# Kernel tuning notes

Hardware: AMD Instinct MI355X
Metric: run time of the kernel (lower is better)

## Reference

```python
import jax, jax.numpy as jnp
import numpy as np

B, L = 4, 2048
D_MODEL, D_STATE, D_CONV, EXPAND = 1024, 16, 4, 2
D_INNER = D_MODEL * EXPAND


def setup_inputs() -> dict:
    key = jax.random.key(0)
    ks = jax.random.split(key, 6)
    x = jax.random.normal(ks[0], (B, L, D_MODEL), dtype=jnp.float32)
    W_in = jax.random.normal(ks[1], (D_MODEL, 2 * D_INNER), dtype=jnp.float32) / np.sqrt(D_MODEL)
    conv_w = jax.random.normal(ks[2], (D_INNER, D_CONV), dtype=jnp.float32) / np.sqrt(D_CONV)
    conv_b = jax.random.normal(ks[3], (D_INNER,), dtype=jnp.float32) * 0.02
    W_x = jax.random.normal(ks[4], (D_INNER, 2 * D_STATE + 1), dtype=jnp.float32) / np.sqrt(D_INNER)
    A_log = jnp.log(jnp.arange(1, D_STATE + 1, dtype=jnp.float32))
    D_param = jnp.ones((D_INNER,), dtype=jnp.float32)
    W_out = jax.random.normal(ks[5], (D_INNER, D_MODEL), dtype=jnp.float32) / np.sqrt(D_INNER)
    return {"x": x, "W_in": W_in, "conv_w": conv_w, "conv_b": conv_b,
            "W_x": W_x, "A_log": A_log, "D_param": D_param, "W_out": W_out}


def _silu(v):
    return v * jax.nn.sigmoid(v)


def reference(x, W_in, conv_w, conv_b, W_x, A_log, D_param, W_out):
    b, l, _ = x.shape
    # input projection and split into ssm branch and gate
    xz = x @ W_in                                   # (b, l, 2*d_inner)
    x_ssm, z = jnp.split(xz, 2, axis=-1)            # each (b, l, d_inner)
    # depthwise causal conv1d (kernel D_CONV, left pad D_CONV-1, truncate to l)
    xp = jnp.pad(x_ssm, ((0, 0), (D_CONV - 1, 0), (0, 0)))
    xc = conv_b
    for k in range(D_CONV):                         # small fixed kernel loop
        xc = xc + xp[:, k:k + l, :] * conv_w[:, k]
    xc = _silu(xc)                                  # (b, l, d_inner)
    # input-dependent delta, B, C
    x_dbl = xc @ W_x                                # (b, l, 2*d_state+1)
    delta = jax.nn.softplus(x_dbl[..., :1])         # (b, l, 1)
    B_mat = x_dbl[..., 1:1 + D_STATE]               # (b, l, n)
    C_mat = x_dbl[..., 1 + D_STATE:]                # (b, l, n)
    A = -jnp.exp(A_log)                             # (n,)
    A_bar = jnp.exp(delta * A)                      # (b, l, n)
    B_bar = delta * B_mat                           # (b, l, n)

    def step(h, inp):
        a, bb, xt, ct = inp                         # (b,n),(b,n),(b,d),(b,n)
        h = a[:, None, :] * h + bb[:, None, :] * xt[:, :, None]  # (b,d,n)
        y = jnp.einsum('bdn,bn->bd', h, ct)
        return h, y

    h0 = jnp.zeros((b, D_INNER, D_STATE), dtype=x.dtype)
    seq = (jnp.swapaxes(A_bar, 0, 1), jnp.swapaxes(B_bar, 0, 1),
           jnp.swapaxes(xc, 0, 1), jnp.swapaxes(C_mat, 0, 1))
    _, ys = jax.lax.scan(step, h0, seq)             # (l, b, d_inner)
    y = jnp.swapaxes(ys, 0, 1)
    y = y + xc * D_param                            # skip connection
    y = y * _silu(z)                                # gating
    return y @ W_out                                # (b, l, d_model)
```

## Files before the change

kernel.cpp:

```cpp
#include <hip/hip_runtime.h>
#include <hip/hip_bf16.h>
#include <math.h>

typedef __hip_bfloat16 bf16;
typedef __attribute__((ext_vector_type(8))) short short8;
typedef __attribute__((ext_vector_type(4))) float f32x4;

#define BATCH   4
#define L_SEQ   2048
#define DMODEL  1024
#define DSTATE  16
#define DCONV   4
#define DINNER  2048
#define M_ROWS  (BATCH * L_SEQ)

#define CHUNK   64
#define NCH     (L_SEQ / CHUNK)
#define PSTR    52
#define NX      33

__device__ __forceinline__ float b2f(bf16 v) { return __bfloat162float(v); }
__device__ __forceinline__ bf16  f2b(float v) { return __float2bfloat16(v); }
__device__ __forceinline__ float us2f(unsigned short u) {
    return __uint_as_float(((unsigned)u) << 16);
}
__device__ __forceinline__ float ldany(const void* p, int i, int f32) {
    return f32 ? ((const float*)p)[i] : b2f(((const bf16*)p)[i]);
}
__device__ __forceinline__ void load_lds16(const void* g, void* l) {
    __builtin_amdgcn_global_load_lds(
        (const __attribute__((address_space(1))) unsigned int*)g,
        (__attribute__((address_space(3))) unsigned int*)l, 16, 0, 0);
}

union V8 { float4 f4; unsigned short us[8]; };

__global__ void detect_dtype(const unsigned int* __restrict__ alog_bits,
                             int* __restrict__ flag)
{
    *flag = (alog_bits[0] == 0u) ? 1 : 0;
}

__global__ __launch_bounds__(256) void convert_bf16(
    const void* __restrict__ src, bf16* __restrict__ dst, int n,
    const int* __restrict__ flag)
{
    const int f = *flag;
    int i = blockIdx.x * 256 + threadIdx.x;
    if (i < n) dst[i] = f2b(ldany(src, i, f));
}

__global__ __launch_bounds__(256) void transpose_any(
    const void* __restrict__ src, bf16* __restrict__ dst,
    int R, int C, const int* __restrict__ flag)
{
    const int f = *flag;
    __shared__ float tile[32][33];
    int tx = threadIdx.x & 31;
    int ty = threadIdx.x >> 5;
    int c0 = blockIdx.x * 32;
    int r0 = blockIdx.y * 32;
    #pragma unroll
    for (int i = 0; i < 4; i++) {
        int r = r0 + ty + i * 8;
        tile[ty + i * 8][tx] = ldany(src, r * C + c0 + tx, f);
    }
    __syncthreads();
    #pragma unroll
    for (int i = 0; i < 4; i++) {
        int cr = c0 + ty + i * 8;
        dst[(size_t)cr * R + r0 + tx] = f2b(tile[tx][ty + i * 8]);
    }
}

__global__ __launch_bounds__(256) void gemm_mfma(
    const bf16* __restrict__ A, const bf16* __restrict__ Bt,
    void* __restrict__ C1, void* __restrict__ C2,
    int M, int N, int K, int split,
    const int* __restrict__ flag, int oMode)
{
    const int fo = (oMode == 2) ? 1 : (oMode & *flag);
    __shared__ __align__(16) bf16 As[128 * 32];
    __shared__ __align__(16) bf16 Bs[128 * 32];
    const int tid  = threadIdx.x;
    const int lane = tid & 63;
    const int w    = tid >> 6;
    const int wr   = w & 1, wc = w >> 1;
    const int m0   = blockIdx.y * 128;
    const int n0   = blockIdx.x * 128;

    f32x4 acc[4][4] = {};

    const int ldr = lane >> 2;
    const int ldc = (lane & 3) * 8;
    const int mrow = lane & 15;
    const int qk   = (lane >> 4) * 8;

    for (int k0 = 0; k0 < K; k0 += 32) {
        __syncthreads();
        #pragma unroll
        for (int j = 0; j < 2; j++) {
            int rg = w * 2 + j;
            int r  = rg * 16 + ldr;
            load_lds16(A  + (size_t)(m0 + r) * K + k0 + ldc, (char*)As + rg * 1024);
            load_lds16(Bt + (size_t)(n0 + r) * K + k0 + ldc, (char*)Bs + rg * 1024);
        }
        __syncthreads();

        short8 af[4], bfr[4];
        #pragma unroll
        for (int i = 0; i < 4; i++) {
            af[i]  = *(const short8*)&As[(wr * 64 + i * 16 + mrow) * 32 + qk];
            bfr[i] = *(const short8*)&Bs[(wc * 64 + i * 16 + mrow) * 32 + qk];
        }
        #pragma unroll
        for (int mi = 0; mi < 4; mi++)
            #pragma unroll
            for (int ni = 0; ni < 4; ni++)
                acc[mi][ni] = __builtin_amdgcn_mfma_f32_16x16x32_bf16(
                    af[mi], bfr[ni], acc[mi][ni], 0, 0, 0);
    }

    const int orow = wr * 64 + (lane >> 4) * 4;
    const int ocol = wc * 64 + (lane & 15);
    #pragma unroll
    for (int mi = 0; mi < 4; mi++)
        #pragma unroll
        for (int ni = 0; ni < 4; ni++)
            #pragma unroll
            for (int r = 0; r < 4; r++) {
                int row = m0 + orow + mi * 16 + r;
                int col = n0 + ocol + ni * 16;
                if (col >= N) continue;
                float v = acc[mi][ni][r];
                if (col < split) {
                    if (fo) ((float*)C1)[(size_t)row * split + col] = v;
                    else    ((bf16*)C1)[(size_t)row * split + col]  = f2b(v);
                } else {
                    int c2 = col - split;
                    if (fo) ((float*)C2)[(size_t)row * (N - split) + c2] = v;
                    else    ((bf16*)C2)[(size_t)row * (N - split) + c2]  = f2b(v);
                }
            }
}

#define CLC 16

__global__ __launch_bounds__(256) void conv_silu_kernel(
    const bf16* __restrict__ x_ssm, const void* __restrict__ conv_w,
    const void* __restrict__ conv_b, bf16* __restrict__ xc,
    const int* __restrict__ flag)
{
    const int f   = *flag;
    const int tid = threadIdx.x;
    const int d0  = tid * 8;
    const int b   = blockIdx.x / (L_SEQ / CLC);
    const int l0  = (blockIdx.x % (L_SEQ / CLC)) * CLC;

    float wk[DCONV][8], bias[8];
    #pragma unroll
    for (int j = 0; j < 8; j++) {
        bias[j] = ldany(conv_b, d0 + j, f);
        #pragma unroll
        for (int k = 0; k < DCONV; k++)
            wk[k][j] = ldany(conv_w, (d0 + j) * DCONV + k, f);
    }

    const size_t rowstr = DINNER;
    const unsigned short* xin = (const unsigned short*)x_ssm;

    float win[3][8];
    #pragma unroll
    for (int r = 0; r < 3; r++) {
        int l = l0 - 3 + r;
        if (l >= 0) {
            V8 v; v.f4 = *(const float4*)(xin + ((size_t)(b * L_SEQ + l)) * rowstr + d0);
            #pragma unroll
            for (int j = 0; j < 8; j++) win[r][j] = us2f(v.us[j]);
        } else {
            #pragma unroll
            for (int j = 0; j < 8; j++) win[r][j] = 0.f;
        }
    }

    #pragma unroll
    for (int t = 0; t < CLC; t++) {
        int l = l0 + t;
        V8 v; v.f4 = *(const float4*)(xin + ((size_t)(b * L_SEQ + l)) * rowstr + d0);
        float cur[8];
        #pragma unroll
        for (int j = 0; j < 8; j++) cur[j] = us2f(v.us[j]);

        V8 o;
        #pragma unroll
        for (int j = 0; j < 8; j++) {
            float s = bias[j];
            s = fmaf(wk[0][j], win[0][j], s);
            s = fmaf(wk[1][j], win[1][j], s);
            s = fmaf(wk[2][j], win[2][j], s);
            s = fmaf(wk[3][j], cur[j],    s);
            float sv = s / (1.f + __expf(-s));
            o.us[j] = (unsigned short)(__bfloat16_as_ushort(f2b(sv)));
        }
        *(float4*)((unsigned short*)xc + ((size_t)(b * L_SEQ + l)) * rowstr + d0) = o.f4;

        #pragma unroll
        for (int j = 0; j < 8; j++) {
            win[0][j] = win[1][j];
            win[1][j] = win[2][j];
            win[2][j] = cur[j];
        }
    }
}

__global__ void transpose_wx(const void* __restrict__ W_x, bf16* __restrict__ W_xT,
                             const int* __restrict__ flag)
{
    const int f = *flag;
    int idx = blockIdx.x * 256 + threadIdx.x;
    if (idx >= NX * DINNER) return;
    int n = idx / DINNER;
    int k = idx - n * DINNER;
    W_xT[idx] = f2b(ldany(W_x, k * NX + n, f));
}

__global__ __launch_bounds__(256) void pack_P(
    const float* __restrict__ xdbl, const void* __restrict__ A_log,
    float* __restrict__ P, const int* __restrict__ flag)
{
    const int f = *flag;
    int i  = blockIdx.x * 256 + threadIdx.x;
    int bl = i >> 4, n = i & 15;
    const float* row = xdbl + (size_t)bl * NX;
    float x0 = row[0];
    float delta = (x0 > 20.f) ? x0 : log1pf(expf(x0));
    float Aneg = -expf(ldany(A_log, n, f));
    float* p = P + (size_t)bl * PSTR;
    p[n]      = expf(delta * Aneg);
    p[16 + n] = delta * row[1 + n];
    p[32 + n] = row[17 + n];
    if (n == 0) p[48] = delta;
}

__global__ __launch_bounds__(256) void scan_phase1(
    const float* __restrict__ P, const bf16* __restrict__ xc,
    float* __restrict__ hstate)
{
    const int blk = blockIdx.x;
    const int b = blk >> 8;
    const int c = (blk >> 3) & 31;
    const int g = blk & 7;
    const int tid = threadIdx.x;
    const int d = g * 256 + tid;

    __shared__ __align__(16) float sP[CHUNK][PSTR];
    __shared__ __align__(16) unsigned short sX[CHUNK][256];

    const float4* psrc = (const float4*)(P + ((size_t)(b * L_SEQ) + c * CHUNK) * PSTR);
    float4* pdst = (float4*)&sP[0][0];
    #pragma unroll
    for (int r = 0; r < 4; r++) {
        int i = r * 256 + tid;
        if (i < (CHUNK * PSTR) / 4) pdst[i] = psrc[i];
    }
    #pragma unroll
    for (int r = 0; r < 16; r++) {
        int i = r * 256 + tid;
        int t = i >> 6;
        int dd = (i & 63) * 4;
        *(ushort4*)&sX[t][dd] = *(const ushort4*)((const unsigned short*)xc +
            ((size_t)(b * L_SEQ) + c * CHUNK + t) * DINNER + g * 256 + dd);
    }
    __syncthreads();

    float h[16];
    #pragma unroll
    for (int n = 0; n < 16; n++) h[n] = 0.f;

    for (int t = 0; t < CHUNK; t++) {
        float xv = us2f(sX[t][tid]);
        float4 a0 = *(const float4*)&sP[t][0];
        float4 a1 = *(const float4*)&sP[t][4];
        float4 a2 = *(const float4*)&sP[t][8];
        float4 a3 = *(const float4*)&sP[t][12];
        float4 b0 = *(const float4*)&sP[t][16];
        float4 b1 = *(const float4*)&sP[t][20];
        float4 b2 = *(const float4*)&sP[t][24];
        float4 b3 = *(const float4*)&sP[t][28];
        float av[16] = {a0.x,a0.y,a0.z,a0.w, a1.x,a1.y,a1.z,a1.w,
                        a2.x,a2.y,a2.z,a2.w, a3.x,a3.y,a3.z,a3.w};
        float bv[16] = {b0.x,b0.y,b0.z,b0.w, b1.x,b1.y,b1.z,b1.w,
                        b2.x,b2.y,b2.z,b2.w, b3.x,b3.y,b3.z,b3.w};
        #pragma unroll
        for (int n = 0; n < 16; n++)
            h[n] = fmaf(av[n], h[n], bv[n] * xv);
    }
    float* out = hstate + (((size_t)b * NCH + c) * DINNER + d) * 16;
    #pragma unroll
    for (int q = 0; q < 4; q++)
        *(float4*)&out[q * 4] = *(const float4*)&h[q * 4];
}

__global__ void sum_delta(const float* __restrict__ P, float* __restrict__ S)
{
    int i = threadIdx.x;
    const float* p = P + ((size_t)((i >> 5) * L_SEQ) + (i & 31) * CHUNK) * PSTR + 48;
    float s = 0.f;
    for (int t = 0; t < CHUNK; t++) s += p[(size_t)t * PSTR];
    S[i] = s;
}

__global__ __launch_bounds__(256) void scan_phase2(
    float* __restrict__ hstate, const float* __restrict__ S,
    const void* __restrict__ A_log, const int* __restrict__ flag)
{
    const int f = *flag;
    const int b = blockIdx.x >> 7;
    const int dg = blockIdx.x & 127;
    const int tid = threadIdx.x;
    const int d = dg * 16 + (tid >> 4);
    const int n = tid & 15;
    const float Aneg = -expf(ldany(A_log, n, f));

    __shared__ float sS[NCH];
    if (tid < NCH) sS[tid] = S[b * NCH + tid];
    __syncthreads();

    float H = 0.f;
    size_t base = ((size_t)b * NCH * DINNER + d) * 16 + n;
    for (int c = 0; c < NCH; c++) {
        size_t idx = base + (size_t)c * (DINNER * 16);
        float hend = hstate[idx];
        hstate[idx] = H;
        H = fmaf(__expf(Aneg * sS[c]), H, hend);
    }
}

__global__ __launch_bounds__(256) void scan_phase3(
    const float* __restrict__ P, const bf16* __restrict__ xc,
    const bf16* __restrict__ z, const void* __restrict__ Dp,
    const float* __restrict__ hstate, bf16* __restrict__ y,
    const int* __restrict__ flag)
{
    const int f = *flag;
    const int blk = blockIdx.x;
    const int b = blk >> 8;
    const int c = (blk >> 3) & 31;
    const int g = blk & 7;
    const int tid = threadIdx.x;
    const int d = g * 256 + tid;

    __shared__ __align__(16) float sP[CHUNK][PSTR];
    __shared__ __align__(16) unsigned short sX[CHUNK][256];

    const float4* psrc = (const float4*)(P + ((size_t)(b * L_SEQ) + c * CHUNK) * PSTR);
    float4* pdst = (float4*)&sP[0][0];
    #pragma unroll
    for (int r = 0; r < 4; r++) {
        int i = r * 256 + tid;
        if (i < (CHUNK * PSTR) / 4) pdst[i] = psrc[i];
    }
    #pragma unroll
    for (int r = 0; r < 16; r++) {
        int i = r * 256 + tid;
        int t = i >> 6;
        int dd = (i & 63) * 4;
        *(ushort4*)&sX[t][dd] = *(const ushort4*)((const unsigned short*)xc +
            ((size_t)(b * L_SEQ) + c * CHUNK + t) * DINNER + g * 256 + dd);
    }
    __syncthreads();

    const float Dd = ldany(Dp, d, f);
    float h[16];
    const float* hin = hstate + (((size_t)b * NCH + c) * DINNER + d) * 16;
    #pragma unroll
    for (int q = 0; q < 4; q++)
        *(float4*)&h[q * 4] = *(const float4*)&hin[q * 4];

    const size_t ybase = ((size_t)(b * L_SEQ) + c * CHUNK) * DINNER + d;
    const unsigned short* zp = (const unsigned short*)z;

    #pragma unroll 4
    for (int t = 0; t < CHUNK; t++) {
        float xv = us2f(sX[t][tid]);
        float4 a0 = *(const float4*)&sP[t][0];
        float4 a1 = *(const float4*)&sP[t][4];
        float4 a2 = *(const float4*)&sP[t][8];
        float4 a3 = *(const float4*)&sP[t][12];
        float4 b0 = *(const float4*)&sP[t][16];
        float4 b1 = *(const float4*)&sP[t][20];
        float4 b2 = *(const float4*)&sP[t][24];
        float4 b3 = *(const float4*)&sP[t][28];
        float4 c0 = *(const float4*)&sP[t][32];
        float4 c1 = *(const float4*)&sP[t][36];
        float4 c2 = *(const float4*)&sP[t][40];
        float4 c3 = *(const float4*)&sP[t][44];
        float av[16] = {a0.x,a0.y,a0.z,a0.w, a1.x,a1.y,a1.z,a1.w,
                        a2.x,a2.y,a2.z,a2.w, a3.x,a3.y,a3.z,a3.w};
        float bv[16] = {b0.x,b0.y,b0.z,b0.w, b1.x,b1.y,b1.z,b1.w,
                        b2.x,b2.y,b2.z,b2.w, b3.x,b3.y,b3.z,b3.w};
        float cv[16] = {c0.x,c0.y,c0.z,c0.w, c1.x,c1.y,c1.z,c1.w,
                        c2.x,c2.y,c2.z,c2.w, c3.x,c3.y,c3.z,c3.w};
        float p0 = 0.f, p1 = 0.f;
        #pragma unroll
        for (int n = 0; n < 16; n += 2) {
            h[n]     = fmaf(av[n],     h[n],     bv[n]     * xv);
            h[n + 1] = fmaf(av[n + 1], h[n + 1], bv[n + 1] * xv);
            p0 = fmaf(h[n],     cv[n],     p0);
            p1 = fmaf(h[n + 1], cv[n + 1], p1);
        }
        float zv = us2f(zp[ybase + (size_t)t * DINNER]);
        float yv = (p0 + p1) + xv * Dd;
        float sz = zv / (1.f + __expf(-zv));
        y[ybase + (size_t)t * DINNER] = f2b(yv * sz);
    }
}

extern "C" void kernel_launch(void* const* d_in, const int* in_sizes, int n_in,
                              void* d_out, int out_size, void* d_ws, size_t ws_size,
                              hipStream_t stream)
{
    const void* x      = d_in[0];
    const void* W_in   = d_in[1];
    const void* conv_w = d_in[2];
    const void* conv_b = d_in[3];
    const void* W_x    = d_in[4];
    const void* A_log  = d_in[5];
    const void* Dp     = d_in[6];
    const void* W_out  = d_in[7];

    char* w = (char*)d_ws;
    bf16* x_ssm = (bf16*)w; w += (size_t)M_ROWS * DINNER * 2;
    bf16* z     = (bf16*)w; w += (size_t)M_ROWS * DINNER * 2;
    bf16* xc    = (bf16*)w; w += (size_t)M_ROWS * DINNER * 2;
    bf16* yb    = (bf16*)w; w += (size_t)M_ROWS * DINNER * 2;
    float* P    = (float*)w; w += (size_t)M_ROWS * PSTR * 4;
    int*  flag  = (int*)w;  w += 256;
    float* S    = (float*)w; w += 4096;

    bf16* x_bf    = yb;
    bf16* W_inT   = xc;
    bf16* W_outT  = x_ssm;
    float* hstate = (float*)((char*)x_ssm + (size_t)DMODEL * DINNER * 2);
    float* xdbl  = (float*)yb;
    bf16*  W_xT  = (bf16*)((char*)yb + 2 * 1024 * 1024);

    detect_dtype<<<1, 1, 0, stream>>>((const unsigned int*)A_log, flag);

    convert_bf16<<<(M_ROWS * DMODEL) / 256, 256, 0, stream>>>(x, x_bf, M_ROWS * DMODEL, flag);
    transpose_any<<<dim3((2 * DINNER) / 32, DMODEL / 32), 256, 0, stream>>>(
        W_in, W_inT, DMODEL, 2 * DINNER, flag);

    gemm_mfma<<<dim3((2 * DINNER) / 128, M_ROWS / 128), 256, 0, stream>>>(
        x_bf, W_inT, x_ssm, z, M_ROWS, 2 * DINNER, DMODEL, DINNER, flag, 0);

    conv_silu_kernel<<<BATCH * (L_SEQ / CLC), 256, 0, stream>>>(
        x_ssm, conv_w, conv_b, xc, flag);

    transpose_any<<<dim3(DMODEL / 32, DINNER / 32), 256, 0, stream>>>(
        W_out, W_outT, DINNER, DMODEL, flag);

    transpose_wx<<<(NX * DINNER + 255) / 256, 256, 0, stream>>>(W_x, W_xT, flag);
    gemm_mfma<<<dim3(1, M_ROWS / 128), 256, 0, stream>>>(
        xc, W_xT, xdbl, xdbl, M_ROWS, NX, DINNER, NX, flag, 2);
    pack_P<<<(M_ROWS * 16) / 256, 256, 0, stream>>>(xdbl, A_log, P, flag);

    scan_phase1<<<BATCH * NCH * 8, 256, 0, stream>>>(P, xc, hstate);
    sum_delta<<<1, BATCH * NCH, 0, stream>>>(P, S);
    scan_phase2<<<BATCH * 128, 256, 0, stream>>>(hstate, S, A_log, flag);
    scan_phase3<<<BATCH * NCH * 8, 256, 0, stream>>>(P, xc, z, Dp, hstate, yb, flag);

    gemm_mfma<<<dim3(DMODEL / 128, M_ROWS / 128), 256, 0, stream>>>(
        yb, W_outT, d_out, d_out, M_ROWS, DMODEL, DINNER, DMODEL, flag, 1);
}
```

Baseline: 454.2 us.

## Split-K the x_dbl GEMM, read scan params from global, parallelize delta sums

The narrow xc@W_x GEMM now splits K four ways into separate fp32 partial buffers, and pack_P sums the partials, so 256 blocks run instead of 64. The scan kernels drop the LDS staging of the per-step parameter rows and read them directly from global memory, which is broadcast across the block. sum_delta becomes one wavefront per chunk with a shuffle reduction, and the GEMM epilogue gets fast paths for tiles that fall wholly on one side of the split. The split-K path adds partial-buffer traffic and an extra reduction, and the global broadcast reads depend on cache behaviour.

After: 408.7 us. 10.0% less time.

```diff
diff --git a/kernel.cpp b/kernel.cpp
--- a/kernel.cpp
+++ b/kernel.cpp
@@ -18,6 +18,7 @@
 #define NCH     (L_SEQ / CHUNK)
 #define PSTR    52
 #define NX      33
+#define KSPL    4
 
 __device__ __forceinline__ float b2f(bf16 v) { return __bfloat162float(v); }
 __device__ __forceinline__ bf16  f2b(float v) { return __float2bfloat16(v); }
@@ -75,9 +76,9 @@
 
 __global__ __launch_bounds__(256) void gemm_mfma(
     const bf16* __restrict__ A, const bf16* __restrict__ Bt,
-    void* __restrict__ C1, void* __restrict__ C2,
-    int M, int N, int K, int split,
-    const int* __restrict__ flag, int oMode)
+    void* __restrict__ C1v, void* __restrict__ C2v,
+    int M, int N, int Kfull, int split,
+    const int* __restrict__ flag, int oMode, int K)
 {
     const int fo = (oMode == 2) ? 1 : (oMode & *flag);
     __shared__ __align__(16) bf16 As[128 * 32];
@@ -88,6 +89,12 @@
     const int wr   = w & 1, wc = w >> 1;
     const int m0   = blockIdx.y * 128;
     const int n0   = blockIdx.x * 128;
+    const int kz   = blockIdx.z;
+    const int kst  = kz * K;
+
+    void* C1 = C1v;
+    void* C2 = C2v;
+    if (kz) { C1 = (char*)C1v + (size_t)kz * M * N * 4; C2 = C1; }
 
     f32x4 acc[4][4] = {};
 
@@ -96,14 +103,14 @@
     const int mrow = lane & 15;
     const int qk   = (lane >> 4) * 8;
 
-    for (int k0 = 0; k0 < K; k0 += 32) {
+    for (int k0 = kst; k0 < kst + K; k0 += 32) {
         __syncthreads();
         #pragma unroll
         for (int j = 0; j < 2; j++) {
             int rg = w * 2 + j;
             int r  = rg * 16 + ldr;
-            load_lds16(A  + (size_t)(m0 + r) * K + k0 + ldc, (char*)As + rg * 1024);
-            load_lds16(Bt + (size_t)(n0 + r) * K + k0 + ldc, (char*)Bs + rg * 1024);
+            load_lds16(A  + (size_t)(m0 + r) * Kfull + k0 + ldc, (char*)As + rg * 1024);
+            load_lds16(Bt + (size_t)(n0 + r) * Kfull + k0 + ldc, (char*)Bs + rg * 1024);
         }
         __syncthreads();
 
@@ -121,27 +128,71 @@
                     af[mi], bfr[ni], acc[mi][ni], 0, 0, 0);
     }
 
-    const int orow = wr * 64 + (lane >> 4) * 4;
+    const int orow = m0 + wr * 64 + (lane >> 4) * 4;
     const int ocol = wc * 64 + (lane & 15);
-    #pragma unroll
-    for (int mi = 0; mi < 4; mi++)
-        #pragma unroll
-        for (int ni = 0; ni < 4; ni++)
-            #pragma unroll
-            for (int r = 0; r < 4; r++) {
-                int row = m0 + orow + mi * 16 + r;
-                int col = n0 + ocol + ni * 16;
-                if (col >= N) continue;
-                float v = acc[mi][ni][r];
-                if (col < split) {
-                    if (fo) ((float*)C1)[(size_t)row * split + col] = v;
-                    else    ((bf16*)C1)[(size_t)row * split + col]  = f2b(v);
-                } else {
-                    int c2 = col - split;
-                    if (fo) ((float*)C2)[(size_t)row * (N - split) + c2] = v;
-                    else    ((bf16*)C2)[(size_t)row * (N - split) + c2]  = f2b(v);
+
+    if (n0 + 128 <= split) {
+        if (fo) {
+            float* Cp = (float*)C1 + (size_t)orow * split + n0 + ocol;
+            #pragma unroll
+            for (int mi = 0; mi < 4; mi++)
+                #pragma unroll
+                for (int ni = 0; ni < 4; ni++)
+                    #pragma unroll
+                    for (int r = 0; r < 4; r++)
+                        Cp[(size_t)(mi * 16 + r) * split + ni * 16] = acc[mi][ni][r];
+        } else {
+            bf16* Cp = (bf16*)C1 + (size_t)orow * split + n0 + ocol;
+            #pragma unroll
+            for (int mi = 0; mi < 4; mi++)
+                #pragma unroll
+                for (int ni = 0; ni < 4; ni++)
+                    #pragma unroll
+                    for (int r = 0; r < 4; r++)
+                        Cp[(size_t)(mi * 16 + r) * split + ni * 16] = f2b(acc[mi][ni][r]);
+        }
+    } else if (n0 >= split) {
+        const int Nc = N - split;
+        if (fo) {
+            float* Cp = (float*)C2 + (size_t)orow * Nc + (n0 - split) + ocol;
+            #pragma unroll
+            for (int mi = 0; mi < 4; mi++)
+                #pragma unroll
+                for (int ni = 0; ni < 4; ni++)
+                    #pragma unroll
+                    for (int r = 0; r < 4; r++)
+                        Cp[(size_t)(mi * 16 + r) * Nc + ni * 16] = acc[mi][ni][r];
+        } else {
+            bf16* Cp = (bf16*)C2 + (size_t)orow * Nc + (n0 - split) + ocol;
+            #pragma unroll
+            for (int mi = 0; mi < 4; mi++)
+                #pragma unroll
+                for (int ni = 0; ni < 4; ni++)
+                    #pragma unroll
+                    for (int r = 0; r < 4; r++)
+                        Cp[(size_t)(mi * 16 + r) * Nc + ni * 16] = f2b(acc[mi][ni][r]);
+        }
+    } else {
+        #pragma unroll
+        for (int mi = 0; mi < 4; mi++)
+            #pragma unroll
+            for (int ni = 0; ni < 4; ni++)
+                #pragma unroll
+                for (int r = 0; r < 4; r++) {
+                    int row = orow + mi * 16 + r;
+                    int col = n0 + ocol + ni * 16;
+                    if (col >= N) continue;
+                    float v = acc[mi][ni][r];
+                    if (col < split) {
+                        if (fo) ((float*)C1)[(size_t)row * split + col] = v;
+                        else    ((bf16*)C1)[(size_t)row * split + col]  = f2b(v);
+                    } else {
+                        int c2 = col - split;
+                        if (fo) ((float*)C2)[(size_t)row * (N - split) + c2] = v;
+                        else    ((bf16*)C2)[(size_t)row * (N - split) + c2]  = f2b(v);
+                    }
                 }
-            }
+    }
 }
 
 #define CLC 16
@@ -231,14 +282,20 @@
     const int f = *flag;
     int i  = blockIdx.x * 256 + threadIdx.x;
     int bl = i >> 4, n = i & 15;
-    const float* row = xdbl + (size_t)bl * NX;
-    float x0 = row[0];
+    float x0 = 0.f, bn = 0.f, cn = 0.f;
+    #pragma unroll
+    for (int s = 0; s < KSPL; s++) {
+        const float* row = xdbl + (size_t)s * M_ROWS * NX + (size_t)bl * NX;
+        x0 += row[0];
+        bn += row[1 + n];
+        cn += row[17 + n];
+    }
     float delta = (x0 > 20.f) ? x0 : log1pf(expf(x0));
     float Aneg = -expf(ldany(A_log, n, f));
     float* p = P + (size_t)bl * PSTR;
     p[n]      = expf(delta * Aneg);
-    p[16 + n] = delta * row[1 + n];
-    p[32 + n] = row[17 + n];
+    p[16 + n] = delta * bn;
+    p[32 + n] = cn;
     if (n == 0) p[48] = delta;
 }
 
@@ -253,16 +310,8 @@
     const int tid = threadIdx.x;
     const int d = g * 256 + tid;
 
-    __shared__ __align__(16) float sP[CHUNK][PSTR];
     __shared__ __align__(16) unsigned short sX[CHUNK][256];
 
-    const float4* psrc = (const float4*)(P + ((size_t)(b * L_SEQ) + c * CHUNK) * PSTR);
-    float4* pdst = (float4*)&sP[0][0];
-    #pragma unroll
-    for (int r = 0; r < 4; r++) {
-        int i = r * 256 + tid;
-        if (i < (CHUNK * PSTR) / 4) pdst[i] = psrc[i];
-    }
     #pragma unroll
     for (int r = 0; r < 16; r++) {
         int i = r * 256 + tid;
@@ -273,20 +322,24 @@
     }
     __syncthreads();
 
+    const float* __restrict__ p = P + ((size_t)(b * L_SEQ) + c * CHUNK) * PSTR;
+
     float h[16];
     #pragma unroll
     for (int n = 0; n < 16; n++) h[n] = 0.f;
 
+    #pragma unroll 4
     for (int t = 0; t < CHUNK; t++) {
+        const float* pt = p + (size_t)t * PSTR;
+        float4 a0 = *(const float4*)(pt + 0);
+        float4 a1 = *(const float4*)(pt + 4);
+        float4 a2 = *(const float4*)(pt + 8);
+        float4 a3 = *(const float4*)(pt + 12);
+        float4 b0 = *(const float4*)(pt + 16);
+        float4 b1 = *(const float4*)(pt + 20);
+        float4 b2 = *(const float4*)(pt + 24);
+        float4 b3 = *(const float4*)(pt + 28);
         float xv = us2f(sX[t][tid]);
-        float4 a0 = *(const float4*)&sP[t][0];
-        float4 a1 = *(const float4*)&sP[t][4];
-        float4 a2 = *(const float4*)&sP[t][8];
-        float4 a3 = *(const float4*)&sP[t][12];
-        float4 b0 = *(const float4*)&sP[t][16];
-        float4 b1 = *(const float4*)&sP[t][20];
-        float4 b2 = *(const float4*)&sP[t][24];
-        float4 b3 = *(const float4*)&sP[t][28];
         float av[16] = {a0.x,a0.y,a0.z,a0.w, a1.x,a1.y,a1.z,a1.w,
                         a2.x,a2.y,a2.z,a2.w, a3.x,a3.y,a3.z,a3.w};
         float bv[16] = {b0.x,b0.y,b0.z,b0.w, b1.x,b1.y,b1.z,b1.w,
@@ -301,13 +354,16 @@
         *(float4*)&out[q * 4] = *(const float4*)&h[q * 4];
 }
 
-__global__ void sum_delta(const float* __restrict__ P, float* __restrict__ S)
-{
-    int i = threadIdx.x;
-    const float* p = P + ((size_t)((i >> 5) * L_SEQ) + (i & 31) * CHUNK) * PSTR + 48;
-    float s = 0.f;
-    for (int t = 0; t < CHUNK; t++) s += p[(size_t)t * PSTR];
-    S[i] = s;
+__global__ __launch_bounds__(64) void sum_delta(const float* __restrict__ P,
+                                                float* __restrict__ S)
+{
+    int i = blockIdx.x;
+    int t = threadIdx.x;
+    float v = P[((size_t)((i >> 5) * L_SEQ) + (i & 31) * CHUNK + t) * PSTR + 48];
+    #pragma unroll
+    for (int off = 32; off > 0; off >>= 1)
+        v += __shfl_xor(v, off);
+    if (t == 0) S[i] = v;
 }
 
 __global__ __launch_bounds__(256) void scan_phase2(
@@ -350,16 +406,8 @@
     const int tid = threadIdx.x;
     const int d = g * 256 + tid;
 
-    __shared__ __align__(16) float sP[CHUNK][PSTR];
     __shared__ __align__(16) unsigned short sX[CHUNK][256];
 
-    const float4* psrc = (const float4*)(P + ((size_t)(b * L_SEQ) + c * CHUNK) * PSTR);
-    float4* pdst = (float4*)&sP[0][0];
-    #pragma unroll
-    for (int r = 0; r < 4; r++) {
-        int i = r * 256 + tid;
-        if (i < (CHUNK * PSTR) / 4) pdst[i] = psrc[i];
-    }
     #pragma unroll
     for (int r = 0; r < 16; r++) {
         int i = r * 256 + tid;
@@ -377,24 +425,26 @@
     for (int q = 0; q < 4; q++)
         *(float4*)&h[q * 4] = *(const float4*)&hin[q * 4];
 
+    const float* __restrict__ p = P + ((size_t)(b * L_SEQ) + c * CHUNK) * PSTR;
     const size_t ybase = ((size_t)(b * L_SEQ) + c * CHUNK) * DINNER + d;
     const unsigned short* zp = (const unsigned short*)z;
 
     #pragma unroll 4
     for (int t = 0; t < CHUNK; t++) {
+        const float* pt = p + (size_t)t * PSTR;
+        float4 a0 = *(const float4*)(pt + 0);
+        float4 a1 = *(const float4*)(pt + 4);
+        float4 a2 = *(const float4*)(pt + 8);
+        float4 a3 = *(const float4*)(pt + 12);
+        float4 b0 = *(const float4*)(pt + 16);
+        float4 b1 = *(const float4*)(pt + 20);
+        float4 b2 = *(const float4*)(pt + 24);
+        float4 b3 = *(const float4*)(pt + 28);
+        float4 c0 = *(const float4*)(pt + 32);
+        float4 c1 = *(const float4*)(pt + 36);
+        float4 c2 = *(const float4*)(pt + 40);
+        float4 c3 = *(const float4*)(pt + 44);
         float xv = us2f(sX[t][tid]);
-        float4 a0 = *(const float4*)&sP[t][0];
-        float4 a1 = *(const float4*)&sP[t][4];
-        float4 a2 = *(const float4*)&sP[t][8];
-        float4 a3 = *(const float4*)&sP[t][12];
-        float4 b0 = *(const float4*)&sP[t][16];
-        float4 b1 = *(const float4*)&sP[t][20];
-        float4 b2 = *(const float4*)&sP[t][24];
-        float4 b3 = *(const float4*)&sP[t][28];
-        float4 c0 = *(const float4*)&sP[t][32];
-        float4 c1 = *(const float4*)&sP[t][36];
-        float4 c2 = *(const float4*)&sP[t][40];
-        float4 c3 = *(const float4*)&sP[t][44];
         float av[16] = {a0.x,a0.y,a0.z,a0.w, a1.x,a1.y,a1.z,a1.w,
                         a2.x,a2.y,a2.z,a2.w, a3.x,a3.y,a3.z,a3.w};
         float bv[16] = {b0.x,b0.y,b0.z,b0.w, b1.x,b1.y,b1.z,b1.w,
@@ -443,7 +493,7 @@
     bf16* W_outT  = x_ssm;
     float* hstate = (float*)((char*)x_ssm + (size_t)DMODEL * DINNER * 2);
     float* xdbl  = (float*)yb;
-    bf16*  W_xT  = (bf16*)((char*)yb + 2 * 1024 * 1024);
+    bf16*  W_xT  = (bf16*)((char*)yb + 8 * 1024 * 1024);
 
     detect_dtype<<<1, 1, 0, stream>>>((const unsigned int*)A_log, flag);
 
@@ -452,7 +502,7 @@
         W_in, W_inT, DMODEL, 2 * DINNER, flag);
 
     gemm_mfma<<<dim3((2 * DINNER) / 128, M_ROWS / 128), 256, 0, stream>>>(
-        x_bf, W_inT, x_ssm, z, M_ROWS, 2 * DINNER, DMODEL, DINNER, flag, 0);
+        x_bf, W_inT, x_ssm, z, M_ROWS, 2 * DINNER, DMODEL, DINNER, flag, 0, DMODEL);
 
     conv_silu_kernel<<<BATCH * (L_SEQ / CLC), 256, 0, stream>>>(
         x_ssm, conv_w, conv_b, xc, flag);
@@ -461,15 +511,15 @@
         W_out, W_outT, DINNER, DMODEL, flag);
 
     transpose_wx<<<(NX * DINNER + 255) / 256, 256, 0, stream>>>(W_x, W_xT, flag);
-    gemm_mfma<<<dim3(1, M_ROWS / 128), 256, 0, stream>>>(
-        xc, W_xT, xdbl, xdbl, M_ROWS, NX, DINNER, NX, flag, 2);
+    gemm_mfma<<<dim3(1, M_ROWS / 128, KSPL), 256, 0, stream>>>(
+        xc, W_xT, xdbl, xdbl, M_ROWS, NX, DINNER, NX, flag, 2, DINNER / KSPL);
     pack_P<<<(M_ROWS * 16) / 256, 256, 0, stream>>>(xdbl, A_log, P, flag);
 
     scan_phase1<<<BATCH * NCH * 8, 256, 0, stream>>>(P, xc, hstate);
-    sum_delta<<<1, BATCH * NCH, 0, stream>>>(P, S);
+    sum_delta<<<BATCH * NCH, 64, 0, stream>>>(P, S);
     scan_phase2<<<BATCH * 128, 256, 0, stream>>>(hstate, S, A_log, flag);
     scan_phase3<<<BATCH * NCH * 8, 256, 0, stream>>>(P, xc, z, Dp, hstate, yb, flag);
 
     gemm_mfma<<<dim3(DMODEL / 128, M_ROWS / 128), 256, 0, stream>>>(
-        yb, W_outT, d_out, d_out, M_ROWS, DMODEL, DINNER, DMODEL, flag, 1);
-}
+        yb, W_outT, d_out, d_out, M_ROWS, DMODEL, DINNER, DMODEL, flag, 1, DINNER);
+}
```
